# Kernel optimization log

Hardware: AMD Instinct MI355X
Metric: run time of the kernel (lower is better)

Reference implementation:

```python
import jax, jax.numpy as jnp
import numpy as np

B, S, H, W, C = 1, 42, 42, 42, 96
WS = 7            # window size (cubic)
SHIFT = 3         # cyclic shift
NH = 3            # num heads
HD = C // NH      # head dim = 32
N = WS ** 3       # tokens per window = 343
NW = (S // WS) * (H // WS) * (W // WS)  # 216 windows
SCALE = HD ** -0.5
EPS = 1e-5


def _rel_pos_index():
    # exact replica of the torch buffer construction (meshgrid 'ij')
    coords = np.stack(np.meshgrid(np.arange(WS), np.arange(WS), np.arange(WS), indexing='ij'))
    flat = coords.reshape(3, -1)                      # (3, N)
    rel = flat[:, :, None] - flat[:, None, :]          # (3, N, N)
    rel = rel.transpose(1, 2, 0).astype(np.int64)      # (N, N, 3)
    rel[..., 0] += WS - 1
    rel[..., 1] += WS - 1
    rel[..., 2] += WS - 1
    rel[..., 0] *= 3 * WS - 1
    rel[..., 1] *= 2 * WS - 1
    return jnp.asarray(rel.sum(-1))                    # (N, N) int

REL_IDX = _rel_pos_index()


def _layernorm(x, w, b):
    mu = jnp.mean(x, -1, keepdims=True)
    var = jnp.mean(jnp.square(x - mu), -1, keepdims=True)
    return (x - mu) * jax.lax.rsqrt(var + EPS) * w + b


def setup_inputs() -> dict:
    key = jax.random.key(0)
    ks = jax.random.split(key, 8)
    std = 0.02
    return {
        'x': jax.random.normal(ks[0], (B, S * H * W, C), jnp.float32),
        'mask_matrix': jnp.zeros((NW, N, N), jnp.float32),
        'norm1_w': jnp.ones((C,), jnp.float32),
        'norm1_b': jnp.zeros((C,), jnp.float32),
        'qkv_w': jax.random.normal(ks[1], (C, 3 * C), jnp.float32) * std,
        'qkv_b': jnp.zeros((3 * C,), jnp.float32),
        'proj_w': jax.random.normal(ks[2], (C, C), jnp.float32) * std,
        'proj_b': jnp.zeros((C,), jnp.float32),
        'rpb_table': jax.random.normal(ks[3], ((2 * WS - 1) ** 3, NH), jnp.float32) * std,
        'norm2_w': jnp.ones((C,), jnp.float32),
        'norm2_b': jnp.zeros((C,), jnp.float32),
        'fc1_w': jax.random.normal(ks[4], (C, 4 * C), jnp.float32) * std,
        'fc1_b': jnp.zeros((4 * C,), jnp.float32),
        'fc2_w': jax.random.normal(ks[5], (4 * C, C), jnp.float32) * std,
        'fc2_b': jnp.zeros((C,), jnp.float32),
    }


def _block(x, mask, norm1_w, norm1_b, qkv_w, qkv_b, proj_w, proj_b,
           rpb_table, norm2_w, norm2_b, fc1_w, fc1_b, fc2_w, fc2_b):
    shortcut = x
    h = _layernorm(x, norm1_w, norm1_b).reshape(B, S, H, W, C)
    # cyclic shift (S,H,W divisible by WS -> no padding needed)
    h = jnp.roll(h, shift=(-SHIFT, -SHIFT, -SHIFT), axis=(1, 2, 3))
    # window partition -> (B*nW, N, C)
    h = h.reshape(B, S // WS, WS, H // WS, WS, W // WS, WS, C)
    h = h.transpose(0, 1, 3, 5, 2, 4, 6, 7).reshape(-1, N, C)
    B_ = h.shape[0]  # B * NW
    # attention
    qkv = (h @ qkv_w + qkv_b).reshape(B_, N, 3, NH, HD).transpose(2, 0, 3, 1, 4)
    q, k, v = qkv[0] * SCALE, qkv[1], qkv[2]
    attn = jnp.einsum('bhnd,bhmd->bhnm', q, k)           # (B_, NH, N, N)
    bias = rpb_table[REL_IDX.reshape(-1)].reshape(N, N, NH).transpose(2, 0, 1)
    attn = attn + bias[None]
    attn = attn.reshape(B, NW, NH, N, N) + mask[None, :, None]
    attn = jax.nn.softmax(attn.reshape(B_, NH, N, N), axis=-1)
    out = jnp.einsum('bhnm,bhmd->bhnd', attn, v).transpose(0, 2, 1, 3).reshape(B_, N, C)
    out = out @ proj_w + proj_b
    # window reverse + reverse shift
    out = out.reshape(B, S // WS, H // WS, W // WS, WS, WS, WS, C)
    out = out.transpose(0, 1, 4, 2, 5, 3, 6, 7).reshape(B, S, H, W, C)
    out = jnp.roll(out, shift=(SHIFT, SHIFT, SHIFT), axis=(1, 2, 3)).reshape(B, S * H * W, C)
    x = shortcut + out
    # MLP with exact (erf) GELU, matching nn.GELU default
    m = _layernorm(x, norm2_w, norm2_b)
    m = jax.nn.gelu(m @ fc1_w + fc1_b, approximate=False) @ fc2_w + fc2_b
    return x + m


def reference(x, mask_matrix, norm1_w, norm1_b, qkv_w, qkv_b, proj_w, proj_b,
              rpb_table, norm2_w, norm2_b, fc1_w, fc1_b, fc2_w, fc2_b):
    return _block(x, mask_matrix, norm1_w, norm1_b, qkv_w, qkv_b, proj_w, proj_b,
                  rpb_table, norm2_w, norm2_b, fc1_w, fc1_b, fc2_w, fc2_b)
```

## Files before the change

kernel.cpp:

```cpp
#include <hip/hip_runtime.h>
#include <hip/hip_bf16.h>
#include <math.h>

#define SDIM 42
#define CDIM 96
#define NTOK 74088
#define NWIN 216
#define NSEQ 343
#define NTOT 7112448
#define QK_SCALE 0.17677669529663687f
#define LN_EPS 1e-5f

typedef short short8 __attribute__((ext_vector_type(8)));
typedef float f32x4 __attribute__((ext_vector_type(4)));
typedef unsigned eu4 __attribute__((ext_vector_type(4)));
union I4S8 { int4 i; short8 s; };

__device__ __forceinline__ int tok_index(int w, int n) {
    int wq = w / 36;
    int wrem = w - wq * 36;
    int wh = wrem / 6;
    int ww = wrem - wh * 6;
    int ps = n / 49;
    int prem = n - ps * 49;
    int ph = prem / 7;
    int pw = prem - ph * 7;
    int s = wq * 7 + ps + 3; if (s >= SDIM) s -= SDIM;
    int h = wh * 7 + ph + 3; if (h >= SDIM) h -= SDIM;
    int c = ww * 7 + pw + 3; if (c >= SDIM) c -= SDIM;
    return (s * SDIM + h) * SDIM + c;
}

__device__ __forceinline__ unsigned pk2(float a, float b) {
    unsigned ua = (unsigned)__bfloat16_as_ushort(__float2bfloat16(a));
    unsigned ub = (unsigned)__bfloat16_as_ushort(__float2bfloat16(b));
    return ua | (ub << 16);
}

__device__ __forceinline__ float fast_erf(float x) {
    float ax = fabsf(x);
    float t = 1.0f / (1.0f + 0.3275911f * ax);
    float y = t*(0.254829592f + t*(-0.284496736f +
              t*(1.421413741f + t*(-1.453152027f + t*1.061405429f))));
    float r = 1.0f - y * __expf(-ax*ax);
    return copysignf(r, x);
}
__device__ __forceinline__ float gelu(float v) {
    return 0.5f * v * (1.0f + fast_erf(v * 0.70710678118654752f));
}

__global__ __launch_bounds__(384) void k_wcast(
    const float* __restrict__ w1, const float* __restrict__ w2,
    const float* __restrict__ pw, const float* __restrict__ qkvw,
    __hip_bfloat16* __restrict__ w1t, __hip_bfloat16* __restrict__ w2t,
    __hip_bfloat16* __restrict__ pwt, __hip_bfloat16* __restrict__ qkvt,
    unsigned* __restrict__ mflag)
{
    int b = blockIdx.x, t = threadIdx.x;
    if (b < 384) {
        if (t < 96) w1t[(size_t)b*96 + t] = __float2bfloat16(w1[(size_t)t*384 + b]);
    } else if (b < 480) {
        int r = b - 384;
        w2t[(size_t)r*384 + t] = __float2bfloat16(w2[(size_t)t*96 + r]);
    } else if (b < 576) {
        int r = b - 480;
        if (t < 96) pwt[(size_t)r*96 + t] = __float2bfloat16(pw[(size_t)t*96 + r]);
    } else if (b < 864) {
        int c = b - 576;
        if (t < 96) qkvt[(size_t)c*96 + t] = __float2bfloat16(qkvw[(size_t)t*288 + c]);
    } else {
        if (t < NWIN) mflag[t] = 0;
    }
}

__global__ __launch_bounds__(256) void k_fused_prep(
    const float* __restrict__ x,
    const float* __restrict__ n1w, const float* __restrict__ n1b,
    const __hip_bfloat16* __restrict__ qkvt, const float* __restrict__ qkvb,
    __hip_bfloat16* __restrict__ qb, __hip_bfloat16* __restrict__ kb,
    __hip_bfloat16* __restrict__ vb,
    const float* __restrict__ mask, unsigned* __restrict__ mflag,
    const float* __restrict__ rpb, float* __restrict__ bg)
{
    __shared__ __align__(16) __hip_bfloat16 sX[64*104];
    const int b = blockIdx.x;
    const int tid = threadIdx.x;

    if (b >= 2160) {
        const int p = b - 2160;
        const int m = p % NSEQ, hh = p / NSEQ;
        const int a0 = m / 49, ar = m - a0*49, a1 = ar / 7, a2 = ar - a1*7;
        for (int n = tid; n < NSEQ; n += 256) {
            int b0 = n / 49, br = n - b0*49, b1 = br / 7, b2 = br - b1*7;
            int idx = (a0 - b0 + 6)*20 + (a1 - b1 + 6)*13 + (a2 - b2 + 6);
            bg[((size_t)hh*NSEQ + m)*NSEQ + n] = rpb[idx*3 + hh];
        }
        return;
    }
    if (b >= 1296) {
        const int idx = b - 1296;
        const int w = idx >> 2, part = idx & 3;
        const unsigned* p = (const unsigned*)(mask + (size_t)w * NSEQ * NSEQ);
        const eu4* p4 = (const eu4*)p;
        unsigned acc = 0;
        const int lo = part * 7353, hi = lo + 7353;
        for (int i = lo + tid; i < hi; i += 256) {
            eu4 v = __builtin_nontemporal_load(p4 + i);
            acc |= (v[0] << 1) | (v[1] << 1) | (v[2] << 1) | (v[3] << 1);
        }
        if (part == 3 && tid == 0) acc |= (p[NSEQ*NSEQ - 1] << 1);
        if (__any(acc != 0) && (tid & 63) == 0) atomicOr(&mflag[w], 1u);
        return;
    }

    const int w  = b / 6;
    const int n0 = (b - w*6) * 64;
    const int g = tid >> 5, l = tid & 31;
    {
        const float lw0 = n1w[l], lw1 = n1w[l+32], lw2 = n1w[l+64];
        const float lb0 = n1b[l], lb1 = n1b[l+32], lb2 = n1b[l+64];
        for (int rr = 0; rr < 8; ++rr) {
            int row = g * 8 + rr;
            int n = n0 + row;
            if (n < NSEQ) {
                const float* xr = x + (size_t)tok_index(w, n) * CDIM;
                float x0 = __builtin_nontemporal_load(xr + l);
                float x1 = __builtin_nontemporal_load(xr + l + 32);
                float x2 = __builtin_nontemporal_load(xr + l + 64);
                float s = x0 + x1 + x2;
                #pragma unroll
                for (int m = 16; m; m >>= 1) s += __shfl_xor(s, m, 32);
                float mu = s * (1.0f/96.0f);
                float d0 = x0-mu, d1 = x1-mu, d2 = x2-mu;
                float vv = d0*d0 + d1*d1 + d2*d2;
                #pragma unroll
                for (int m = 16; m; m >>= 1) vv += __shfl_xor(vv, m, 32);
                float rstd = rsqrtf(vv * (1.0f/96.0f) + LN_EPS);
                sX[row*104 + l]    = __float2bfloat16(d0 * rstd * lw0 + lb0);
                sX[row*104 + l+32] = __float2bfloat16(d1 * rstd * lw1 + lb1);
                sX[row*104 + l+64] = __float2bfloat16(d2 * rstd * lw2 + lb2);
            } else {
                sX[row*104 + l]    = __float2bfloat16(0.f);
                sX[row*104 + l+32] = __float2bfloat16(0.f);
                sX[row*104 + l+64] = __float2bfloat16(0.f);
            }
        }
    }
    __syncthreads();

    const int wv = tid >> 6, lane = tid & 63;
    const int l15 = lane & 15, h = lane >> 4;
    const int trow = wv*16 + l15;
    const int n = n0 + trow;

    I4S8 bx[3];
    #pragma unroll
    for (int ks = 0; ks < 3; ++ks)
        bx[ks].i = *(const int4*)&sX[trow*104 + ks*32 + h*8];

    for (int nt = 0; nt < 18; ++nt) {
        f32x4 acc = {0.f,0.f,0.f,0.f};
        #pragma unroll
        for (int ks = 0; ks < 3; ++ks) {
            I4S8 af;
            af.i = *(const int4*)(qkvt + (size_t)(nt*16 + l15)*96 + ks*32 + h*8);
            acc = __builtin_amdgcn_mfma_f32_16x16x32_bf16(af.s, bx[ks].s, acc, 0, 0, 0);
        }
        if (n < NSEQ) {
            const int colbase = nt*16 + 4*h;
            const int sel = colbase / 96;
            const int rem = colbase - sel*96;
            const int head = rem >> 5, d0 = rem & 31;
            float4 bb = *(const float4*)&qkvb[colbase];
            float v0 = acc[0] + bb.x, v1 = acc[1] + bb.y;
            float v2 = acc[2] + bb.z, v3 = acc[3] + bb.w;
            if (sel == 0) { v0 *= QK_SCALE; v1 *= QK_SCALE; v2 *= QK_SCALE; v3 *= QK_SCALE; }
            __hip_bfloat16* dst = (sel == 0 ? qb : (sel == 1 ? kb : vb));
            *(uint2*)&dst[(((size_t)w*3 + head)*NSEQ + n)*32 + d0] =
                make_uint2(pk2(v0, v1), pk2(v2, v3));
        }
    }
}

template<bool UM>
__device__ __forceinline__ void attn_qloop(
    const __hip_bfloat16* __restrict__ qb, const float* __restrict__ bg,
    const float* __restrict__ mask, __hip_bfloat16* __restrict__ aob,
    const __hip_bfloat16* sK, const __hip_bfloat16* sVT,
    size_t base, int w, int head, int wid, int l15, int h)
{
    for (int mt = wid; mt < 22; mt += 8) {
        const int m = mt*16 + l15;
        const int mc = (m < NSEQ) ? m : (NSEQ-1);

        I4S8 qf;
        qf.i = *(const int4*)(qb + base + (size_t)mc*32 + h*8);

        const float* mrow = mask + ((size_t)w*NSEQ + mc)*NSEQ;
        const float* brow = bg   + ((size_t)head*NSEQ + mc)*NSEQ;

        float lsum = 0.f;
        f32x4 acc0 = {0.f,0.f,0.f,0.f}, acc1 = {0.f,0.f,0.f,0.f};

        auto step = [&](int t, float4 mkA, float4 bsA, float4 mkB, float4 bsB) {
            float p[8];
            {
                I4S8 kf;
                kf.i = *(const int4*)&sK[(t*16 + l15)*32 + h*8];
                f32x4 st = __builtin_amdgcn_mfma_f32_16x16x32_bf16(
                    kf.s, qf.s, (f32x4){0.f,0.f,0.f,0.f}, 0, 0, 0);
                if constexpr (UM) {
                    p[0] = __expf(st[0] + mkA.x + bsA.x);
                    p[1] = __expf(st[1] + mkA.y + bsA.y);
                    p[2] = __expf(st[2] + mkA.z + bsA.z);
                    p[3] = __expf(st[3] + mkA.w + bsA.w);
                } else {
                    p[0] = __expf(st[0] + bsA.x);
                    p[1] = __expf(st[1] + bsA.y);
                    p[2] = __expf(st[2] + bsA.z);
                    p[3] = __expf(st[3] + bsA.w);
                }
                lsum += (p[0] + p[1]) + (p[2] + p[3]);
            }
            {
                I4S8 kf;
                kf.i = *(const int4*)&sK[((t+1)*16 + l15)*32 + h*8];
                f32x4 st = __builtin_amdgcn_mfma_f32_16x16x32_bf16(
                    kf.s, qf.s, (f32x4){0.f,0.f,0.f,0.f}, 0, 0, 0);
                if constexpr (UM) {
                    p[4] = __expf(st[0] + mkB.x + bsB.x);
                    p[5] = __expf(st[1] + mkB.y + bsB.y);
                    p[6] = __expf(st[2] + mkB.z + bsB.z);
                    p[7] = __expf(st[3] + mkB.w + bsB.w);
                } else {
                    p[4] = __expf(st[0] + bsB.x);
                    p[5] = __expf(st[1] + bsB.y);
                    p[6] = __expf(st[2] + bsB.z);
                    p[7] = __expf(st[3] + bsB.w);
                }
                lsum += (p[4] + p[5]) + (p[6] + p[7]);
            }
            I4S8 pf;
            pf.i = make_int4(pk2(p[0], p[1]), pk2(p[2], p[3]),
                             pk2(p[4], p[5]), pk2(p[6], p[7]));
            const int vcol = t*16 + 4*h;
            uint2 va0 = *(const uint2*)&sVT[(l15     )*372 + vcol];
            uint2 vb0 = *(const uint2*)&sVT[(l15     )*372 + vcol + 16];
            uint2 va1 = *(const uint2*)&sVT[(16 + l15)*372 + vcol];
            uint2 vb1 = *(const uint2*)&sVT[(16 + l15)*372 + vcol + 16];
            I4S8 vf0; vf0.i = make_int4(va0.x, va0.y, vb0.x, vb0.y);
            I4S8 vf1; vf1.i = make_int4(va1.x, va1.y, vb1.x, vb1.y);
            acc0 = __builtin_amdgcn_mfma_f32_16x16x32_bf16(vf0.s, pf.s, acc0, 0, 0, 0);
            acc1 = __builtin_amdgcn_mfma_f32_16x16x32_bf16(vf1.s, pf.s, acc1, 0, 0, 0);
        };

        const float4 z4 = {0.f,0.f,0.f,0.f};
        float4 mkA = UM ? *(const float4*)&mrow[4*h]      : z4;
        float4 bsA =      *(const float4*)&brow[4*h];
        float4 mkB = UM ? *(const float4*)&mrow[16 + 4*h] : z4;
        float4 bsB =      *(const float4*)&brow[16 + 4*h];

        #pragma unroll 1
        for (int c = 0; c < 9; ++c) {
            const int nb = (2*c + 2)*16 + 4*h;
            float4 nmkA = UM ? *(const float4*)&mrow[nb]      : z4;
            float4 nbsA =      *(const float4*)&brow[nb];
            float4 nmkB = UM ? *(const float4*)&mrow[nb + 16] : z4;
            float4 nbsB =      *(const float4*)&brow[nb + 16];
            step(2*c, mkA, bsA, mkB, bsB);
            mkA = nmkA; bsA = nbsA; mkB = nmkB; bsB = nbsB;
        }

        {
            float4 nmkA = UM ? *(const float4*)&mrow[320 + 4*h] : z4;
            float4 nbsA =      *(const float4*)&brow[320 + 4*h];
            float4 nmkB = z4, nbsB;
            {
                const int nb = 336 + 4*h;
                int i0 = nb,   c0 = (i0 < NSEQ) ? i0 : (NSEQ-1);
                int i1 = nb+1, c1 = (i1 < NSEQ) ? i1 : (NSEQ-1);
                int i2 = nb+2, c2 = (i2 < NSEQ) ? i2 : (NSEQ-1);
                int i3 = nb+3, c3 = (i3 < NSEQ) ? i3 : (NSEQ-1);
                if constexpr (UM) {
                    nmkB.x = mrow[c0]; nmkB.y = mrow[c1];
                    nmkB.z = mrow[c2]; nmkB.w = mrow[c3];
                }
                nbsB.x = brow[c0]; nbsB.y = brow[c1];
                nbsB.z = brow[c2]; nbsB.w = brow[c3];
            }
            step(18, mkA, bsA, mkB, bsB);
            mkA = nmkA; bsA = nbsA; mkB = nmkB; bsB = nbsB;
        }

        {
            float p[8];
            {
                I4S8 kf;
                kf.i = *(const int4*)&sK[(20*16 + l15)*32 + h*8];
                f32x4 st = __builtin_amdgcn_mfma_f32_16x16x32_bf16(
                    kf.s, qf.s, (f32x4){0.f,0.f,0.f,0.f}, 0, 0, 0);
                if constexpr (UM) {
                    p[0] = __expf(st[0] + mkA.x + bsA.x);
                    p[1] = __expf(st[1] + mkA.y + bsA.y);
                    p[2] = __expf(st[2] + mkA.z + bsA.z);
                    p[3] = __expf(st[3] + mkA.w + bsA.w);
                } else {
                    p[0] = __expf(st[0] + bsA.x);
                    p[1] = __expf(st[1] + bsA.y);
                    p[2] = __expf(st[2] + bsA.z);
                    p[3] = __expf(st[3] + bsA.w);
                }
                lsum += (p[0] + p[1]) + (p[2] + p[3]);
            }
            {
                I4S8 kf;
                kf.i = *(const int4*)&sK[(21*16 + l15)*32 + h*8];
                f32x4 st = __builtin_amdgcn_mfma_f32_16x16x32_bf16(
                    kf.s, qf.s, (f32x4){0.f,0.f,0.f,0.f}, 0, 0, 0);
                float sb[4];
                if constexpr (UM) {
                    sb[0] = mkB.x + bsB.x; sb[1] = mkB.y + bsB.y;
                    sb[2] = mkB.z + bsB.z; sb[3] = mkB.w + bsB.w;
                } else {
                    sb[0] = bsB.x; sb[1] = bsB.y; sb[2] = bsB.z; sb[3] = bsB.w;
                }
                const int nb = 336 + 4*h;
                #pragma unroll
                for (int r = 0; r < 4; ++r) {
                    const int nn = nb + r;
                    float e = 0.f;
                    if (nn < NSEQ) e = __expf(st[r] + sb[r]);
                    p[4+r] = e; lsum += e;
                }
            }
            I4S8 pf;
            pf.i = make_int4(pk2(p[0], p[1]), pk2(p[2], p[3]),
                             pk2(p[4], p[5]), pk2(p[6], p[7]));
            const int vcol = 320 + 4*h;
            uint2 va0 = *(const uint2*)&sVT[(l15     )*372 + vcol];
            uint2 vb0 = *(const uint2*)&sVT[(l15     )*372 + vcol + 16];
            uint2 va1 = *(const uint2*)&sVT[(16 + l15)*372 + vcol];
            uint2 vb1 = *(const uint2*)&sVT[(16 + l15)*372 + vcol + 16];
            I4S8 vf0; vf0.i = make_int4(va0.x, va0.y, vb0.x, vb0.y);
            I4S8 vf1; vf1.i = make_int4(va1.x, va1.y, vb1.x, vb1.y);
            acc0 = __builtin_amdgcn_mfma_f32_16x16x32_bf16(vf0.s, pf.s, acc0, 0, 0, 0);
            acc1 = __builtin_amdgcn_mfma_f32_16x16x32_bf16(vf1.s, pf.s, acc1, 0, 0, 0);
        }

        lsum += __shfl_xor(lsum, 16, 64);
        lsum += __shfl_xor(lsum, 32, 64);
        const float inv = 1.0f / lsum;

        if (m < NSEQ) {
            __hip_bfloat16* orow = &aob[((size_t)w*NSEQ + m)*CDIM + head*32];
            *(uint2*)&orow[4*h] =
                make_uint2(pk2(acc0[0]*inv, acc0[1]*inv), pk2(acc0[2]*inv, acc0[3]*inv));
            *(uint2*)&orow[16 + 4*h] =
                make_uint2(pk2(acc1[0]*inv, acc1[1]*inv), pk2(acc1[2]*inv, acc1[3]*inv));
        }
    }
}

__global__ __launch_bounds__(512) void k_attn(
    const __hip_bfloat16* __restrict__ qb, const __hip_bfloat16* __restrict__ kb,
    const __hip_bfloat16* __restrict__ vb, const float* __restrict__ bg,
    const float* __restrict__ mask, const unsigned* __restrict__ mflag,
    __hip_bfloat16* __restrict__ aob)
{
    __shared__ __hip_bfloat16 sK[352*32];
    __shared__ __hip_bfloat16 sVT[32*372];
    const int tid = threadIdx.x;
    const int v = blockIdx.x;
    const int xcd = v & 7, tt = v >> 3;
    const int j = tt / 3, head = tt - 3*j;
    const int w = xcd + 8*j;
    const size_t base = ((size_t)w*3 + head) * (NSEQ*32);

    {
        const int4* ksrc = (const int4*)(kb + base);
        for (int i = tid; i < NSEQ*4; i += 512) {
            int row = i >> 2, q = i & 3;
            *(int4*)&sK[row*32 + q*8] = ksrc[i];
        }
        const int4* vsrc = (const int4*)(vb + base);
        for (int i = tid; i < NSEQ*4; i += 512) {
            int n = i >> 2, dc = i & 3;
            int4 t = vsrc[i];
            const __hip_bfloat16* tp = (const __hip_bfloat16*)&t;
            #pragma unroll
            for (int k2 = 0; k2 < 8; ++k2) sVT[(dc*8 + k2)*372 + n] = tp[k2];
        }
        for (int i = tid; i < 32*29; i += 512) {
            int d = i / 29, n = NSEQ + (i - d*29);
            sVT[d*372 + n] = __float2bfloat16(0.f);
        }
    }
    __syncthreads();

    const int wid = tid >> 6, lane = tid & 63;
    const int l15 = lane & 15, h = lane >> 4;

    if (mflag[w] == 0)
        attn_qloop<false>(qb, bg, mask, aob, sK, sVT, base, w, head, wid, l15, h);
    else
        attn_qloop<true>(qb, bg, mask, aob, sK, sVT, base, w, head, wid, l15, h);
}

__global__ __launch_bounds__(256) void k_pmlp(
    const __hip_bfloat16* __restrict__ aob, const __hip_bfloat16* __restrict__ pwt,
    const float* __restrict__ pb, const float* __restrict__ x,
    const float* __restrict__ n2w, const float* __restrict__ n2b,
    const __hip_bfloat16* __restrict__ w1t, const float* __restrict__ b1,
    const __hip_bfloat16* __restrict__ w2t, const float* __restrict__ b2,
    float* __restrict__ out)
{
    __shared__ __align__(16) __hip_bfloat16 sBuf[64*104];
    __shared__ __align__(16) __hip_bfloat16 sW[2][96*100];
    const int w = blockIdx.y;
    const int n0 = blockIdx.x * 64;
    const int tid = threadIdx.x;
    const int wv = tid >> 6, lane = tid & 63;
    const int l15 = lane & 15, h = lane >> 4;
    const int trow = wv*16 + l15;
    const int n = n0 + trow;
    const int nc = (n < NSEQ) ? n : (NSEQ-1);
    const int tok = tok_index(w, nc);

    uint2 st[9];
    auto stage_load = [&](const __hip_bfloat16* src, int stride) {
        #pragma unroll
        for (int r = 0; r < 9; ++r) {
            int i = tid + r*256;
            int row = i / 24, cb = i - row*24;
            st[r] = *(const uint2*)(src + (size_t)row*stride + cb*4);
        }
    };
    auto stage_write = [&](int buf) {
        #pragma unroll
        for (int r = 0; r < 9; ++r) {
            int i = tid + r*256;
            int row = i / 24, cb = i - row*24;
            *(uint2*)&sW[buf][row*100 + cb*4] = st[r];
        }
    };

    stage_load(pwt, 96);
    I4S8 bm[3];
    #pragma unroll
    for (int ks = 0; ks < 3; ++ks)
        bm[ks].i = *(const int4*)(aob + ((size_t)w*NSEQ + nc)*CDIM + ks*32 + h*8);
    stage_write(0);
    __syncthreads();

    stage_load(w1t, 96);
    float4 x1v[6];
    #pragma unroll
    for (int nt = 0; nt < 6; ++nt) {
        f32x4 acc = {0.f,0.f,0.f,0.f};
        #pragma unroll
        for (int ks = 0; ks < 3; ++ks) {
            I4S8 af;
            af.i = *(const int4*)&sW[0][(nt*16 + l15)*100 + ks*32 + h*8];
            acc = __builtin_amdgcn_mfma_f32_16x16x32_bf16(af.s, bm[ks].s, acc, 0, 0, 0);
        }
        const int col = nt*16 + 4*h;
        float4 xr = *(const float4*)&x[(size_t)tok*CDIM + col];
        float4 bb = *(const float4*)&pb[col];
        x1v[nt].x = xr.x + acc[0] + bb.x;
        x1v[nt].y = xr.y + acc[1] + bb.y;
        x1v[nt].z = xr.z + acc[2] + bb.z;
        x1v[nt].w = xr.w + acc[3] + bb.w;
    }
    {
        float s = 0.f, q = 0.f;
        #pragma unroll
        for (int nt = 0; nt < 6; ++nt) {
            s += (x1v[nt].x + x1v[nt].y) + (x1v[nt].z + x1v[nt].w);
            q += (x1v[nt].x*x1v[nt].x + x1v[nt].y*x1v[nt].y)
               + (x1v[nt].z*x1v[nt].z + x1v[nt].w*x1v[nt].w);
        }
        s += __shfl_xor(s, 16, 64); s += __shfl_xor(s, 32, 64);
        q += __shfl_xor(q, 16, 64); q += __shfl_xor(q, 32, 64);
        float mu = s * (1.0f/96.0f);
        float var = q * (1.0f/96.0f) - mu*mu;
        float rstd = rsqrtf(var + LN_EPS);
        #pragma unroll
        for (int nt = 0; nt < 6; ++nt) {
            const int col = nt*16 + 4*h;
            float4 nwv = *(const float4*)&n2w[col];
            float4 nbv = *(const float4*)&n2b[col];
            float a0 = (x1v[nt].x - mu)*rstd*nwv.x + nbv.x;
            float a1 = (x1v[nt].y - mu)*rstd*nwv.y + nbv.y;
            float a2 = (x1v[nt].z - mu)*rstd*nwv.z + nbv.z;
            float a3 = (x1v[nt].w - mu)*rstd*nwv.w + nbv.w;
            *(uint2*)&sBuf[trow*104 + col] = make_uint2(pk2(a0, a1), pk2(a2, a3));
        }
    }
    I4S8 bx[3];
    #pragma unroll
    for (int ks = 0; ks < 3; ++ks)
        bx[ks].i = *(const int4*)&sBuf[trow*104 + ks*32 + h*8];
    stage_write(1);
    __syncthreads();

    f32x4 accs[6];
    #pragma unroll
    for (int nt = 0; nt < 6; ++nt) accs[nt] = (f32x4){0.f,0.f,0.f,0.f};

    #pragma unroll 1
    for (int q = 0; q < 4; ++q) {
        stage_load(w2t + q*96, 384);
        #pragma unroll
        for (int ntl = 0; ntl < 6; ++ntl) {
            I4S8 af[3];
            #pragma unroll
            for (int ks = 0; ks < 3; ++ks)
                af[ks].i = *(const int4*)&sW[1][(ntl*16 + l15)*100 + ks*32 + h*8];
            f32x4 acc = {0.f,0.f,0.f,0.f};
            #pragma unroll
            for (int ks = 0; ks < 3; ++ks)
                acc = __builtin_amdgcn_mfma_f32_16x16x32_bf16(af[ks].s, bx[ks].s, acc, 0, 0, 0);
            float4 bb = *(const float4*)&b1[q*96 + ntl*16 + 4*h];
            *(uint2*)&sBuf[trow*104 + ntl*16 + 4*h] =
                make_uint2(pk2(gelu(acc[0]+bb.x), gelu(acc[1]+bb.y)),
                           pk2(gelu(acc[2]+bb.z), gelu(acc[3]+bb.w)));
        }
        stage_write(0);
        __syncthreads();

        if (q < 3) stage_load(w1t + (size_t)(q+1)*96*96, 96);
        #pragma unroll
        for (int ksl = 0; ksl < 3; ++ksl) {
            I4S8 bmq;
            bmq.i = *(const int4*)&sBuf[trow*104 + ksl*32 + h*8];
            #pragma unroll
            for (int nt = 0; nt < 6; ++nt) {
                I4S8 af;
                af.i = *(const int4*)&sW[0][(nt*16 + l15)*100 + ksl*32 + h*8];
                accs[nt] = __builtin_amdgcn_mfma_f32_16x16x32_bf16(af.s, bmq.s, accs[nt], 0, 0, 0);
            }
        }
        if (q < 3) {
            stage_write(1);
            __syncthreads();
        }
    }

    if (n < NSEQ) {
        #pragma unroll
        for (int nt = 0; nt < 6; ++nt) {
            const int col = nt*16 + 4*h;
            float4 bb = *(const float4*)&b2[col];
            float4 o;
            o.x = x1v[nt].x + accs[nt][0] + bb.x;
            o.y = x1v[nt].y + accs[nt][1] + bb.y;
            o.z = x1v[nt].z + accs[nt][2] + bb.z;
            o.w = x1v[nt].w + accs[nt][3] + bb.w;
            *(float4*)&out[(size_t)tok*CDIM + col] = o;
        }
    }
}

extern "C" void kernel_launch(void* const* d_in, const int* in_sizes, int n_in,
                              void* d_out, int out_size, void* d_ws, size_t ws_size,
                              hipStream_t stream) {
    const float* x    = (const float*)d_in[0];
    const float* mask = (const float*)d_in[1];
    const float* n1w  = (const float*)d_in[2];
    const float* n1b  = (const float*)d_in[3];
    const float* qkvw = (const float*)d_in[4];
    const float* qkvb = (const float*)d_in[5];
    const float* pw   = (const float*)d_in[6];
    const float* pb   = (const float*)d_in[7];
    const float* rpb  = (const float*)d_in[8];
    const float* n2w  = (const float*)d_in[9];
    const float* n2b  = (const float*)d_in[10];
    const float* w1   = (const float*)d_in[11];
    const float* b1   = (const float*)d_in[12];
    const float* w2   = (const float*)d_in[13];
    const float* b2   = (const float*)d_in[14];
    float* out = (float*)d_out;

    __hip_bfloat16* qb  = (__hip_bfloat16*)d_ws;
    __hip_bfloat16* kb  = qb + NTOT;
    __hip_bfloat16* vb  = kb + NTOT;
    __hip_bfloat16* aob = vb + NTOT;
    float* bg = (float*)(aob + NTOT);
    __hip_bfloat16* w1t  = (__hip_bfloat16*)(bg + 352948);
    __hip_bfloat16* w2t  = w1t + 384*96;
    __hip_bfloat16* pwt  = w2t + 96*384;
    __hip_bfloat16* qkvt = pwt + 96*96;
    unsigned* mflag = (unsigned*)(qkvt + 288*96);

    hipLaunchKernelGGL(k_wcast, dim3(865), dim3(384), 0, stream,
                       w1, w2, pw, qkvw, w1t, w2t, pwt, qkvt, mflag);
    hipLaunchKernelGGL(k_fused_prep, dim3(1296 + 4*NWIN + NSEQ*3), dim3(256), 0, stream,
                       x, n1w, n1b, qkvt, qkvb, qb, kb, vb, mask, mflag, rpb, bg);
    hipLaunchKernelGGL(k_attn, dim3(NWIN*3), dim3(512), 0, stream,
                       qb, kb, vb, bg, mask, mflag, aob);
    hipLaunchKernelGGL(k_pmlp, dim3(6, NWIN), dim3(256), 0, stream,
                       aob, pwt, pb, x, n2w, n2b, w1t, b1, w2t, b2, out);
}
```

Before: 164.6 us.

## Halve weight staging tiles in proj+MLP kernel to cut LDS and registers

The proj+MLP kernel now stages weights in 48-row half tiles instead of full 96-row tiles. This halves the shared weight buffer and the per-thread staging registers, which can raise occupancy. In exchange it doubles the number of stage/sync phases per fc1/fc2 chunk, adding barriers and giving each phase less MFMA work to hide global loads behind.

```diff
diff --git a/kernel.cpp b/kernel.cpp
--- a/kernel.cpp
+++ b/kernel.cpp
@@ -415,7 +415,7 @@
     float* __restrict__ out)
 {
     __shared__ __align__(16) __hip_bfloat16 sBuf[64*104];
-    __shared__ __align__(16) __hip_bfloat16 sW[2][96*100];
+    __shared__ __align__(16) __hip_bfloat16 sW[2][48*100];
     const int w = blockIdx.y;
     const int n0 = blockIdx.x * 64;
     const int tid = threadIdx.x;
@@ -426,41 +426,66 @@
     const int nc = (n < NSEQ) ? n : (NSEQ-1);
     const int tok = tok_index(w, nc);
 
-    uint2 st[9];
-    auto stage_load = [&](const __hip_bfloat16* src, int stride) {
-        #pragma unroll
-        for (int r = 0; r < 9; ++r) {
+    uint2 st[5];
+    auto stageL = [&](const __hip_bfloat16* src, int stride, int rowoff) {
+        #pragma unroll
+        for (int r = 0; r < 5; ++r) {
             int i = tid + r*256;
-            int row = i / 24, cb = i - row*24;
-            st[r] = *(const uint2*)(src + (size_t)row*stride + cb*4);
+            if (i < 1152) {
+                int row = i / 24, cb = i - row*24;
+                st[r] = *(const uint2*)(src + (size_t)(rowoff + row)*stride + cb*4);
+            }
         }
     };
-    auto stage_write = [&](int buf) {
-        #pragma unroll
-        for (int r = 0; r < 9; ++r) {
+    auto stageW = [&](int buf) {
+        #pragma unroll
+        for (int r = 0; r < 5; ++r) {
             int i = tid + r*256;
-            int row = i / 24, cb = i - row*24;
-            *(uint2*)&sW[buf][row*100 + cb*4] = st[r];
+            if (i < 1152) {
+                int row = i / 24, cb = i - row*24;
+                *(uint2*)&sW[buf][row*100 + cb*4] = st[r];
+            }
         }
     };
 
-    stage_load(pwt, 96);
+    stageL(pwt, 96, 0);
     I4S8 bm[3];
     #pragma unroll
     for (int ks = 0; ks < 3; ++ks)
         bm[ks].i = *(const int4*)(aob + ((size_t)w*NSEQ + nc)*CDIM + ks*32 + h*8);
-    stage_write(0);
+    stageW(0);
     __syncthreads();
 
-    stage_load(w1t, 96);
     float4 x1v[6];
+    stageL(pwt, 96, 48);
     #pragma unroll
-    for (int nt = 0; nt < 6; ++nt) {
+    for (int nt = 0; nt < 3; ++nt) {
         f32x4 acc = {0.f,0.f,0.f,0.f};
         #pragma unroll
         for (int ks = 0; ks < 3; ++ks) {
             I4S8 af;
             af.i = *(const int4*)&sW[0][(nt*16 + l15)*100 + ks*32 + h*8];
+            acc = __builtin_amdgcn_mfma_f32_16x16x32_bf16(af.s, bm[ks].s, acc, 0, 0, 0);
+        }
+        const int col = nt*16 + 4*h;
+        float4 xr = *(const float4*)&x[(size_t)tok*CDIM + col];
+        float4 bb = *(const float4*)&pb[col];
+        x1v[nt].x = xr.x + acc[0] + bb.x;
+        x1v[nt].y = xr.y + acc[1] + bb.y;
+        x1v[nt].z = xr.z + acc[2] + bb.z;
+        x1v[nt].w = xr.w + acc[3] + bb.w;
+    }
+    stageW(1);
+    __syncthreads();
+
+    stageL(w1t, 96, 0);
+    #pragma unroll
+    for (int nt = 3; nt < 6; ++nt) {
+        f32x4 acc = {0.f,0.f,0.f,0.f};
+        #pragma unroll
+        for (int ks = 0; ks < 3; ++ks) {
+            I4S8 af;
+            af.i = *(const int4*)&sW[1][((nt-3)*16 + l15)*100 + ks*32 + h*8];
             acc = __builtin_amdgcn_mfma_f32_16x16x32_bf16(af.s, bm[ks].s, acc, 0, 0, 0);
         }
         const int col = nt*16 + 4*h;
@@ -500,50 +525,79 @@
     #pragma unroll
     for (int ks = 0; ks < 3; ++ks)
         bx[ks].i = *(const int4*)&sBuf[trow*104 + ks*32 + h*8];
-    stage_write(1);
+    stageW(0);
     __syncthreads();
 
     f32x4 accs[6];
     #pragma unroll
     for (int nt = 0; nt < 6; ++nt) accs[nt] = (f32x4){0.f,0.f,0.f,0.f};
 
+    int buf = 0;
     #pragma unroll 1
     for (int q = 0; q < 4; ++q) {
-        stage_load(w2t + q*96, 384);
-        #pragma unroll
-        for (int ntl = 0; ntl < 6; ++ntl) {
+        stageL(w1t, 96, q*96 + 48);
+        #pragma unroll
+        for (int j = 0; j < 3; ++j) {
             I4S8 af[3];
             #pragma unroll
             for (int ks = 0; ks < 3; ++ks)
-                af[ks].i = *(const int4*)&sW[1][(ntl*16 + l15)*100 + ks*32 + h*8];
+                af[ks].i = *(const int4*)&sW[buf][(j*16 + l15)*100 + ks*32 + h*8];
             f32x4 acc = {0.f,0.f,0.f,0.f};
             #pragma unroll
             for (int ks = 0; ks < 3; ++ks)
                 acc = __builtin_amdgcn_mfma_f32_16x16x32_bf16(af[ks].s, bx[ks].s, acc, 0, 0, 0);
-            float4 bb = *(const float4*)&b1[q*96 + ntl*16 + 4*h];
-            *(uint2*)&sBuf[trow*104 + ntl*16 + 4*h] =
+            float4 bb = *(const float4*)&b1[q*96 + j*16 + 4*h];
+            *(uint2*)&sBuf[trow*104 + j*16 + 4*h] =
                 make_uint2(pk2(gelu(acc[0]+bb.x), gelu(acc[1]+bb.y)),
                            pk2(gelu(acc[2]+bb.z), gelu(acc[3]+bb.w)));
         }
-        stage_write(0);
-        __syncthreads();
-
-        if (q < 3) stage_load(w1t + (size_t)(q+1)*96*96, 96);
+        stageW(buf^1); __syncthreads(); buf ^= 1;
+
+        stageL(w2t + q*96, 384, 0);
+        #pragma unroll
+        for (int j = 0; j < 3; ++j) {
+            I4S8 af[3];
+            #pragma unroll
+            for (int ks = 0; ks < 3; ++ks)
+                af[ks].i = *(const int4*)&sW[buf][(j*16 + l15)*100 + ks*32 + h*8];
+            f32x4 acc = {0.f,0.f,0.f,0.f};
+            #pragma unroll
+            for (int ks = 0; ks < 3; ++ks)
+                acc = __builtin_amdgcn_mfma_f32_16x16x32_bf16(af[ks].s, bx[ks].s, acc, 0, 0, 0);
+            float4 bb = *(const float4*)&b1[q*96 + (j+3)*16 + 4*h];
+            *(uint2*)&sBuf[trow*104 + (j+3)*16 + 4*h] =
+                make_uint2(pk2(gelu(acc[0]+bb.x), gelu(acc[1]+bb.y)),
+                           pk2(gelu(acc[2]+bb.z), gelu(acc[3]+bb.w)));
+        }
+        stageW(buf^1); __syncthreads(); buf ^= 1;
+
+        stageL(w2t + q*96, 384, 48);
         #pragma unroll
         for (int ksl = 0; ksl < 3; ++ksl) {
             I4S8 bmq;
             bmq.i = *(const int4*)&sBuf[trow*104 + ksl*32 + h*8];
             #pragma unroll
-            for (int nt = 0; nt < 6; ++nt) {
+            for (int j = 0; j < 3; ++j) {
                 I4S8 af;
-                af.i = *(const int4*)&sW[0][(nt*16 + l15)*100 + ksl*32 + h*8];
-                accs[nt] = __builtin_amdgcn_mfma_f32_16x16x32_bf16(af.s, bmq.s, accs[nt], 0, 0, 0);
-            }
-        }
-        if (q < 3) {
-            stage_write(1);
-            __syncthreads();
-        }
+                af.i = *(const int4*)&sW[buf][(j*16 + l15)*100 + ksl*32 + h*8];
+                accs[j] = __builtin_amdgcn_mfma_f32_16x16x32_bf16(af.s, bmq.s, accs[j], 0, 0, 0);
+            }
+        }
+        stageW(buf^1); __syncthreads(); buf ^= 1;
+
+        if (q < 3) stageL(w1t, 96, (q+1)*96);
+        #pragma unroll
+        for (int ksl = 0; ksl < 3; ++ksl) {
+            I4S8 bmq;
+            bmq.i = *(const int4*)&sBuf[trow*104 + ksl*32 + h*8];
+            #pragma unroll
+            for (int j = 0; j < 3; ++j) {
+                I4S8 af;
+                af.i = *(const int4*)&sW[buf][(j*16 + l15)*100 + ksl*32 + h*8];
+                accs[j+3] = __builtin_amdgcn_mfma_f32_16x16x32_bf16(af.s, bmq.s, accs[j+3], 0, 0, 0);
+            }
+        }
+        if (q < 3) { stageW(buf^1); __syncthreads(); buf ^= 1; }
     }
 
     if (n < NSEQ) {
```

Measured after the change: 167.0 us. No clear change (+1.4%).
